# Performance work log

Measured on AMD Instinct MI355X. Metric: run time of the kernel, lower is better.

Reference implementation:

```python
import jax, jax.numpy as jnp
import numpy as np

C_M, C_Z, C, H = 256, 128, 32, 8
N_SEQ, N_RES = 256, 256
EPS = 1e-5


def _layer_norm(x, w, b):
    mu = jnp.mean(x, axis=-1, keepdims=True)
    var = jnp.mean(jnp.square(x - mu), axis=-1, keepdims=True)
    return (x - mu) * jax.lax.rsqrt(var + EPS) * w + b


def setup_inputs() -> dict:
    key = jax.random.key(0)
    ks = jax.random.split(key, 10)
    s = lambda fan_in: 1.0 / np.sqrt(fan_in)
    return {
        "m": jax.random.normal(ks[0], (N_SEQ, N_RES, C_M), jnp.float32),
        "z": jax.random.normal(ks[1], (N_RES, N_RES, C_Z), jnp.float32),
        "ln_m_w": jnp.ones((C_M,), jnp.float32),
        "ln_m_b": jnp.zeros((C_M,), jnp.float32),
        "ln_z_w": jnp.ones((C_Z,), jnp.float32),
        "ln_z_b": jnp.zeros((C_Z,), jnp.float32),
        "w_z": jax.random.normal(ks[2], (C_Z, H), jnp.float32) * s(C_Z),
        "w_q": jax.random.normal(ks[3], (C_M, H * C), jnp.float32) * s(C_M),
        "w_k": jax.random.normal(ks[4], (C_M, H * C), jnp.float32) * s(C_M),
        "w_v": jax.random.normal(ks[5], (C_M, H * C), jnp.float32) * s(C_M),
        "w_g": jax.random.normal(ks[6], (C_M, H * C), jnp.float32) * s(C_M),
        "b_g": jnp.zeros((H * C,), jnp.float32),
        "w_o": jax.random.normal(ks[7], (H * C, C_M), jnp.float32) * s(H * C),
        "b_o": jnp.zeros((C_M,), jnp.float32),
    }


def reference(m, z, ln_m_w, ln_m_b, ln_z_w, ln_z_b, w_z, w_q, w_k, w_v, w_g, b_g, w_o, b_o):
    S, R = m.shape[0], m.shape[1]
    mn = _layer_norm(m, ln_m_w, ln_m_b)                      # (S, R, c_m)
    # pair bias: LN + Linear(c_z -> H), then movedim(-1, -3): (R, R, H) -> (H, R, R)
    bias = jnp.moveaxis(_layer_norm(z, ln_z_w, ln_z_b) @ w_z, -1, -3)

    q = (mn @ w_q).reshape(S, R, H, C)
    k = (mn @ w_k).reshape(S, R, H, C)
    v = (mn @ w_v).reshape(S, R, H, C)

    scale = 1.0 / np.sqrt(C)
    # attention over residue axis (attn_dim=-2); bias broadcast over N_seq
    logits = jnp.einsum("sqhd,skhd->shqk", q, k) * scale + bias[None]  # (S, H, R, R)
    attn = jax.nn.softmax(logits, axis=-1)
    o = jnp.einsum("shqk,skhd->sqhd", attn, v).reshape(S, R, H * C)

    g = jax.nn.sigmoid(mn @ w_g + b_g)                       # (S, R, H*c)
    return (g * o) @ w_o + b_o                               # (S, R, c_m)
```

## Files before the change

kernel.cpp:

```cpp
#include <hip/hip_runtime.h>
#include <hip/hip_bf16.h>

typedef __hip_bfloat16 bf16;
typedef __attribute__((ext_vector_type(8))) short short8;
typedef __attribute__((ext_vector_type(16))) float f32x16;

#define NS 256
#define NR 256
#define CM 256
#define CZ 128
#define NH 8
#define CH 32
#define LN_EPS 1e-5f
#define LOG2E 1.4426950408889634f
#define SCALE2 (0.17677669529663687f * 1.4426950408889634f)

__device__ __forceinline__ unsigned pk_bf16(float lo, float hi) {
  unsigned r;
  asm volatile("v_cvt_pk_bf16_f32 %0, %1, %2" : "=v"(r) : "v"(lo), "v"(hi));
  return r;
}

__device__ __forceinline__ short8 load8(const bf16* p) {
  return __builtin_bit_cast(short8, *(const uint4*)p);
}

__global__ __launch_bounds__(256) void pack_w_kernel(
    const float* __restrict__ wq, const float* __restrict__ wk,
    const float* __restrict__ wv, const float* __restrict__ wg,
    const float* __restrict__ wo, bf16* __restrict__ dst) {
  int mat = blockIdx.y;
  const float* src = mat == 0 ? wq : mat == 1 ? wk : mat == 2 ? wv
                   : mat == 3 ? wg : wo;
  float sc = (mat == 0) ? SCALE2 : 1.0f;
  int t = blockIdx.x * 256 + threadIdx.x;
  int n = t & 255;
  int hi = (t >> 8) & 1;
  int kc = t >> 9;
  int kbase = kc * 16 + hi * 8;
  bf16 tmp[8];
  #pragma unroll
  for (int j = 0; j < 8; ++j)
    tmp[j] = __float2bfloat16(src[(size_t)(kbase + j) * 256 + n] * sc);
  *(uint4*)(dst + (size_t)mat * 65536 +
            ((size_t)(kc * 2 + hi) * 256 + n) * 8) = *(const uint4*)tmp;
}

__global__ __launch_bounds__(256) void ln_m_kernel(
    const float* __restrict__ m, const float* __restrict__ w,
    const float* __restrict__ b, bf16* __restrict__ mn) {
  int row = blockIdx.x * 4 + (threadIdx.x >> 6);
  int lane = threadIdx.x & 63;

  float4 x = ((const float4*)(m + (size_t)row * CM))[lane];
  float sum = x.x + x.y + x.z + x.w;
  #pragma unroll
  for (int off = 32; off; off >>= 1) sum += __shfl_xor(sum, off);
  float mu = sum * (1.0f / CM);

  float dx = x.x - mu, dy = x.y - mu, dz = x.z - mu, dw = x.w - mu;
  float ss = dx * dx + dy * dy + dz * dz + dw * dw;
  #pragma unroll
  for (int off = 32; off; off >>= 1) ss += __shfl_xor(ss, off);
  float rs = rsqrtf(ss * (1.0f / CM) + LN_EPS);

  float4 wv = ((const float4*)w)[lane];
  float4 bv = ((const float4*)b)[lane];
  unsigned p0 = pk_bf16(dx * rs * wv.x + bv.x, dy * rs * wv.y + bv.y);
  unsigned p1 = pk_bf16(dz * rs * wv.z + bv.z, dw * rs * wv.w + bv.w);
  uint2 u;
  u.x = p0;
  u.y = p1;
  *(uint2*)(mn + (size_t)row * CM + lane * 4) = u;
}

__global__ __launch_bounds__(128) void bias_kernel(
    const float* __restrict__ z, const float* __restrict__ w,
    const float* __restrict__ b, const float* __restrict__ wz,
    float* __restrict__ biasP) {
  int row = blockIdx.x;
  int t = threadIdx.x;
  __shared__ float red[2];
  __shared__ float zn[CZ];
  __shared__ float part[16][9];

  float x = z[(size_t)row * CZ + t];

  float v = x;
  #pragma unroll
  for (int off = 32; off; off >>= 1) v += __shfl_xor(v, off);
  if ((t & 63) == 0) red[t >> 6] = v;
  __syncthreads();
  float mu = (red[0] + red[1]) * (1.0f / CZ);
  float d = x - mu;
  __syncthreads();

  v = d * d;
  #pragma unroll
  for (int off = 32; off; off >>= 1) v += __shfl_xor(v, off);
  if ((t & 63) == 0) red[t >> 6] = v;
  __syncthreads();
  float var = (red[0] + red[1]) * (1.0f / CZ);

  zn[t] = d * rsqrtf(var + LN_EPS) * w[t] + b[t];
  __syncthreads();

  int h = t & 7, grp = t >> 3;
  float acc = 0.0f;
  #pragma unroll
  for (int cc = 0; cc < 8; ++cc) {
    int c = grp * 8 + cc;
    acc += zn[c] * wz[c * NH + h];
  }
  part[grp][h] = acc;
  __syncthreads();

  if (t < NH) {
    float s = 0.0f;
    #pragma unroll
    for (int g = 0; g < 16; ++g) s += part[g][t];
    int i = row >> 8, j = row & 255;
    int qt = i >> 5, lo = i & 31;
    int tt = j >> 5, rem = j & 31;
    int hi2 = (rem >> 2) & 1;
    int r = ((rem >> 3) << 2) | (rem & 3);
    biasP[(((size_t)t * 8 + qt) * 128 + tt * 16 + r) * 64 + hi2 * 32 + lo] =
        s * LOG2E;
  }
}

__global__ __launch_bounds__(256, 2) void qkvg_mfma_kernel(
    const bf16* __restrict__ mn, const bf16* __restrict__ wp,
    const float* __restrict__ bg,
    bf16* __restrict__ qo, bf16* __restrict__ ko,
    bf16* __restrict__ vo, bf16* __restrict__ go) {
  int mat = threadIdx.x >> 6;
  int lane = threadIdx.x & 63;
  int lo = lane & 31, hi = lane >> 5;
  size_t m0 = (size_t)blockIdx.x * 32;

  const bf16* arow = mn + (m0 + lo) * 256 + hi * 8;
  const bf16* wbase = wp + (size_t)mat * 65536 + ((size_t)hi * 256 + lo) * 8;

  f32x16 acc[8] = {};
  #pragma unroll 2
  for (int kc = 0; kc < 16; ++kc) {
    short8 a = load8(arow + kc * 16);
    const bf16* wkc = wbase + (size_t)kc * 4096;
    #pragma unroll
    for (int nt = 0; nt < 8; ++nt) {
      short8 b = load8(wkc + nt * 256);
      acc[nt] = __builtin_amdgcn_mfma_f32_32x32x16_bf16(a, b, acc[nt], 0, 0, 0);
    }
  }

  bf16* outp = mat == 0 ? qo : mat == 1 ? ko : mat == 2 ? vo : go;
  if (mat == 3) {
    #pragma unroll
    for (int nt = 0; nt < 8; ++nt) {
      float bgv = bg[nt * 32 + lo];
      #pragma unroll
      for (int r = 0; r < 16; ++r) {
        int crow = (r & 3) + ((r >> 2) << 3) + (hi << 2);
        float sv = 1.0f / (1.0f + __expf(-(acc[nt][r] + bgv)));
        outp[(m0 + crow) * 256 + nt * 32 + lo] = __float2bfloat16(sv);
      }
    }
  } else {
    #pragma unroll
    for (int nt = 0; nt < 8; ++nt) {
      #pragma unroll
      for (int r = 0; r < 16; ++r) {
        int crow = (r & 3) + ((r >> 2) << 3) + (hi << 2);
        outp[(m0 + crow) * 256 + nt * 32 + lo] = __float2bfloat16(acc[nt][r]);
      }
    }
  }
}

__global__ __launch_bounds__(256) void transpose_v_kernel(
    const bf16* __restrict__ vo, bf16* __restrict__ vT) {
  int s = blockIdx.x >> 3, h = blockIdx.x & 7;
  int t = threadIdx.x;
  __shared__ bf16 tile[256][40];

  #pragma unroll
  for (int p = 0; p < 4; ++p) {
    int k = p * 64 + (t >> 2);
    int c0 = (t & 3) * 8;
    uint4 u = *(const uint4*)(vo + ((size_t)(s * 256 + k)) * 256 + h * 32 + c0);
    *(uint4*)&tile[k][c0] = u;
  }
  __syncthreads();

  int c = t >> 3, k0 = (t & 7) * 32;
  bf16 buf[32];
  #pragma unroll
  for (int j = 0; j < 32; ++j) buf[j] = tile[k0 + j][c];
  bf16* dst = vT + (((size_t)(s * 8 + h) * 32 + c) * 256 + k0);
  #pragma unroll
  for (int q = 0; q < 4; ++q)
    *(uint4*)(dst + q * 8) = *(const uint4*)(buf + q * 8);
}

__global__ __launch_bounds__(256, 2) void attn_mfma_kernel(
    const bf16* __restrict__ qb, const bf16* __restrict__ kb,
    const bf16* __restrict__ vT, const bf16* __restrict__ gb,
    const float* __restrict__ biasP, bf16* __restrict__ gob) {
  int wb = (blockIdx.x & 7) * 512 + (blockIdx.x >> 3);
  int wid = wb * 4 + (threadIdx.x >> 6);
  int lane = threadIdx.x & 63;
  int lo = lane & 31;
  int hi = lane >> 5;
  int s = wid >> 6;
  int h = (wid >> 3) & 7;
  int qt = wid & 7;
  int q0 = qt * 32;

  const size_t base = (size_t)s * NR * 256 + h * CH;

  const float* bp = biasP + (((size_t)h * 8 + qt) * 128) * 64 + lane;

  short8 qf[2];
  #pragma unroll
  for (int cc = 0; cc < 2; ++cc)
    qf[cc] = load8(qb + base + (size_t)(q0 + lo) * 256 + cc * 16 + hi * 8);

  f32x16 acc[8];
  __builtin_amdgcn_s_setprio(1);
  #pragma unroll
  for (int t = 0; t < 8; ++t) {
    short8 kf0 = load8(kb + base + (size_t)(t * 32 + lo) * 256 + hi * 8);
    short8 kf1 = load8(kb + base + (size_t)(t * 32 + lo) * 256 + 16 + hi * 8);
    f32x16 z = {};
    acc[t] = __builtin_amdgcn_mfma_f32_32x32x16_bf16(kf0, qf[0], z, 0, 0, 0);
    acc[t] = __builtin_amdgcn_mfma_f32_32x32x16_bf16(kf1, qf[1], acc[t], 0, 0, 0);
  }
  __builtin_amdgcn_s_setprio(0);

  float l0 = 0.0f, l1 = 0.0f, l2 = 0.0f, l3 = 0.0f;
  #pragma unroll
  for (int t = 0; t < 8; ++t) {
    #pragma unroll
    for (int r = 0; r < 16; r += 4) {
      float e0 = exp2f(acc[t][r + 0] + bp[(t * 16 + r + 0) * 64]);
      float e1 = exp2f(acc[t][r + 1] + bp[(t * 16 + r + 1) * 64]);
      float e2 = exp2f(acc[t][r + 2] + bp[(t * 16 + r + 2) * 64]);
      float e3 = exp2f(acc[t][r + 3] + bp[(t * 16 + r + 3) * 64]);
      acc[t][r + 0] = e0;
      acc[t][r + 1] = e1;
      acc[t][r + 2] = e2;
      acc[t][r + 3] = e3;
      l0 += e0;
      l1 += e1;
      l2 += e2;
      l3 += e3;
    }
  }
  float l = (l0 + l1) + (l2 + l3);
  l += __shfl_xor(l, 32);

  f32x16 o = {};
  const bf16* vt = vT + ((size_t)(s * NH + h) * CH + lo) * 256;
  #pragma unroll
  for (int kc = 0; kc < 16; ++kc) {
    int t = kc >> 1;
    int rb = (kc & 1) << 3;
    unsigned uL0 = pk_bf16(acc[t][rb + 0], acc[t][rb + 1]);
    unsigned uL1 = pk_bf16(acc[t][rb + 2], acc[t][rb + 3]);
    unsigned uH0 = pk_bf16(acc[t][rb + 4], acc[t][rb + 5]);
    unsigned uH1 = pk_bf16(acc[t][rb + 6], acc[t][rb + 7]);
    unsigned sL0 = __shfl_xor(uL0, 32), sL1 = __shfl_xor(uL1, 32);
    unsigned sH0 = __shfl_xor(uH0, 32), sH1 = __shfl_xor(uH1, 32);
    uint4 pu;
    pu.x = hi ? sH0 : uL0;
    pu.y = hi ? sH1 : uL1;
    pu.z = hi ? uH0 : sL0;
    pu.w = hi ? uH1 : sL1;
    short8 pf = __builtin_bit_cast(short8, pu);
    short8 vf = load8(vt + kc * 16 + hi * 8);
    o = __builtin_amdgcn_mfma_f32_32x32x16_bf16(pf, vf, o, 0, 0, 0);
  }

  float linv = 1.0f / l;
  #pragma unroll
  for (int r = 0; r < 16; ++r) {
    int crow = (r & 3) + ((r >> 2) << 3) + (hi << 2);
    float li = __shfl(linv, crow);
    size_t idx = base + (size_t)(q0 + crow) * 256 + lo;
    float gg = __bfloat162float(gb[idx]);
    gob[idx] = __float2bfloat16(gg * o[r] * li);
  }
}

__global__ __launch_bounds__(256, 2) void out_mfma_kernel(
    const bf16* __restrict__ gob, const bf16* __restrict__ wop,
    const float* __restrict__ bo, float* __restrict__ out) {
  int wid = blockIdx.x * 4 + (threadIdx.x >> 6);
  int lane = threadIdx.x & 63;
  int lo = lane & 31, hi = lane >> 5;
  size_t m0 = (size_t)wid * 32;

  const bf16* arow = gob + (m0 + lo) * 256 + hi * 8;
  const bf16* wbase = wop + ((size_t)hi * 256 + lo) * 8;

  f32x16 acc[8] = {};
  #pragma unroll 2
  for (int kc = 0; kc < 16; ++kc) {
    short8 a = load8(arow + kc * 16);
    const bf16* wkc = wbase + (size_t)kc * 4096;
    #pragma unroll
    for (int nt = 0; nt < 8; ++nt) {
      short8 b = load8(wkc + nt * 256);
      acc[nt] = __builtin_amdgcn_mfma_f32_32x32x16_bf16(a, b, acc[nt], 0, 0, 0);
    }
  }

  #pragma unroll
  for (int nt = 0; nt < 8; ++nt) {
    float bv = bo[nt * 32 + lo];
    #pragma unroll
    for (int r = 0; r < 16; ++r) {
      int crow = (r & 3) + ((r >> 2) << 3) + (hi << 2);
      out[(m0 + crow) * 256 + nt * 32 + lo] = acc[nt][r] + bv;
    }
  }
}

extern "C" void kernel_launch(void* const* d_in, const int* in_sizes, int n_in,
                              void* d_out, int out_size, void* d_ws, size_t ws_size,
                              hipStream_t stream) {
  const float* m      = (const float*)d_in[0];
  const float* z      = (const float*)d_in[1];
  const float* ln_m_w = (const float*)d_in[2];
  const float* ln_m_b = (const float*)d_in[3];
  const float* ln_z_w = (const float*)d_in[4];
  const float* ln_z_b = (const float*)d_in[5];
  const float* w_z    = (const float*)d_in[6];
  const float* w_q    = (const float*)d_in[7];
  const float* w_k    = (const float*)d_in[8];
  const float* w_v    = (const float*)d_in[9];
  const float* w_g    = (const float*)d_in[10];
  const float* b_g    = (const float*)d_in[11];
  const float* w_o    = (const float*)d_in[12];
  const float* b_o    = (const float*)d_in[13];
  float* out = (float*)d_out;

  const size_t SZ = (size_t)NS * NR * 256;

  bf16* mn   = (bf16*)d_ws;
  bf16* qb   = mn + SZ;
  bf16* kb   = qb + SZ;
  bf16* vo   = kb + SZ;
  bf16* gb   = vo + SZ;
  bf16* gob  = gb + SZ;
  float* biasP = (float*)(gob + SZ);
  bf16* wp   = (bf16*)(biasP + NH * NR * NR);
  bf16* wop  = wp + 4 * 65536;
  bf16* vT   = mn;

  pack_w_kernel<<<dim3(32, 5), 256, 0, stream>>>(w_q, w_k, w_v, w_g, w_o, wp);
  ln_m_kernel<<<(NS * NR) / 4, 256, 0, stream>>>(m, ln_m_w, ln_m_b, mn);
  bias_kernel<<<NR * NR, 128, 0, stream>>>(z, ln_z_w, ln_z_b, w_z, biasP);
  qkvg_mfma_kernel<<<(NS * NR) / 32, 256, 0, stream>>>(mn, wp, b_g,
                                                       qb, kb, vo, gb);
  transpose_v_kernel<<<NS * NH, 256, 0, stream>>>(vo, vT);
  attn_mfma_kernel<<<(NS * NH * 8) / 4, 256, 0, stream>>>(qb, kb, vT, gb,
                                                          biasP, gob);
  out_mfma_kernel<<<(NS * NR) / 32 / 4, 256, 0, stream>>>(gob, wop, b_o, out);
}
```

Before: 311.6 us.

## Split attention into two key halves, vectorize bias loads, raise occupancy

```diff
diff --git a/kernel.cpp b/kernel.cpp
--- a/kernel.cpp
+++ b/kernel.cpp
@@ -124,8 +124,10 @@
     int tt = j >> 5, rem = j & 31;
     int hi2 = (rem >> 2) & 1;
     int r = ((rem >> 3) << 2) | (rem & 3);
-    biasP[(((size_t)t * 8 + qt) * 128 + tt * 16 + r) * 64 + hi2 * 32 + lo] =
-        s * LOG2E;
+    int ifrag = tt * 16 + r;
+    int lane = hi2 * 32 + lo;
+    biasP[((((size_t)t * 8 + qt) * 32 + (ifrag >> 2)) * 64 + lane) * 4 +
+          (ifrag & 3)] = s * LOG2E;
   }
 }
 
@@ -203,7 +205,7 @@
     *(uint4*)(dst + q * 8) = *(const uint4*)(buf + q * 8);
 }
 
-__global__ __launch_bounds__(256, 2) void attn_mfma_kernel(
+__global__ __launch_bounds__(256, 3) void attn_mfma_kernel(
     const bf16* __restrict__ qb, const bf16* __restrict__ kb,
     const bf16* __restrict__ vT, const bf16* __restrict__ gb,
     const float* __restrict__ biasP, bf16* __restrict__ gob) {
@@ -219,70 +221,81 @@
 
   const size_t base = (size_t)s * NR * 256 + h * CH;
 
-  const float* bp = biasP + (((size_t)h * 8 + qt) * 128) * 64 + lane;
+  const float4* bp4 =
+      (const float4*)biasP + ((size_t)(h * 8 + qt) * 32) * 64 + lane;
 
   short8 qf[2];
   #pragma unroll
   for (int cc = 0; cc < 2; ++cc)
     qf[cc] = load8(qb + base + (size_t)(q0 + lo) * 256 + cc * 16 + hi * 8);
 
-  f32x16 acc[8];
-  __builtin_amdgcn_s_setprio(1);
-  #pragma unroll
-  for (int t = 0; t < 8; ++t) {
-    short8 kf0 = load8(kb + base + (size_t)(t * 32 + lo) * 256 + hi * 8);
-    short8 kf1 = load8(kb + base + (size_t)(t * 32 + lo) * 256 + 16 + hi * 8);
-    f32x16 z = {};
-    acc[t] = __builtin_amdgcn_mfma_f32_32x32x16_bf16(kf0, qf[0], z, 0, 0, 0);
-    acc[t] = __builtin_amdgcn_mfma_f32_32x32x16_bf16(kf1, qf[1], acc[t], 0, 0, 0);
-  }
-  __builtin_amdgcn_s_setprio(0);
-
+  const bf16* vt = vT + ((size_t)(s * NH + h) * CH + lo) * 256;
+
+  f32x16 o = {};
   float l0 = 0.0f, l1 = 0.0f, l2 = 0.0f, l3 = 0.0f;
-  #pragma unroll
-  for (int t = 0; t < 8; ++t) {
-    #pragma unroll
-    for (int r = 0; r < 16; r += 4) {
-      float e0 = exp2f(acc[t][r + 0] + bp[(t * 16 + r + 0) * 64]);
-      float e1 = exp2f(acc[t][r + 1] + bp[(t * 16 + r + 1) * 64]);
-      float e2 = exp2f(acc[t][r + 2] + bp[(t * 16 + r + 2) * 64]);
-      float e3 = exp2f(acc[t][r + 3] + bp[(t * 16 + r + 3) * 64]);
-      acc[t][r + 0] = e0;
-      acc[t][r + 1] = e1;
-      acc[t][r + 2] = e2;
-      acc[t][r + 3] = e3;
-      l0 += e0;
-      l1 += e1;
-      l2 += e2;
-      l3 += e3;
-    }
-  }
+
+  #pragma unroll
+  for (int hs = 0; hs < 2; ++hs) {
+    f32x16 acc[4];
+    __builtin_amdgcn_s_setprio(1);
+    #pragma unroll
+    for (int th = 0; th < 4; ++th) {
+      int t = hs * 4 + th;
+      short8 kf0 = load8(kb + base + (size_t)(t * 32 + lo) * 256 + hi * 8);
+      short8 kf1 = load8(kb + base + (size_t)(t * 32 + lo) * 256 + 16 + hi * 8);
+      f32x16 z = {};
+      acc[th] = __builtin_amdgcn_mfma_f32_32x32x16_bf16(kf0, qf[0], z, 0, 0, 0);
+      acc[th] =
+          __builtin_amdgcn_mfma_f32_32x32x16_bf16(kf1, qf[1], acc[th], 0, 0, 0);
+    }
+    __builtin_amdgcn_s_setprio(0);
+
+    #pragma unroll
+    for (int th = 0; th < 4; ++th) {
+      int t = hs * 4 + th;
+      #pragma unroll
+      for (int j = 0; j < 4; ++j) {
+        float4 b4 = bp4[(t * 4 + j) * 64];
+        float e0 = exp2f(acc[th][j * 4 + 0] + b4.x);
+        float e1 = exp2f(acc[th][j * 4 + 1] + b4.y);
+        float e2 = exp2f(acc[th][j * 4 + 2] + b4.z);
+        float e3 = exp2f(acc[th][j * 4 + 3] + b4.w);
+        acc[th][j * 4 + 0] = e0;
+        acc[th][j * 4 + 1] = e1;
+        acc[th][j * 4 + 2] = e2;
+        acc[th][j * 4 + 3] = e3;
+        l0 += e0;
+        l1 += e1;
+        l2 += e2;
+        l3 += e3;
+      }
+    }
+
+    #pragma unroll
+    for (int kc2 = 0; kc2 < 8; ++kc2) {
+      int th = kc2 >> 1;
+      int rb = (kc2 & 1) << 3;
+      unsigned uL0 = pk_bf16(acc[th][rb + 0], acc[th][rb + 1]);
+      unsigned uL1 = pk_bf16(acc[th][rb + 2], acc[th][rb + 3]);
+      unsigned uH0 = pk_bf16(acc[th][rb + 4], acc[th][rb + 5]);
+      unsigned uH1 = pk_bf16(acc[th][rb + 6], acc[th][rb + 7]);
+      unsigned sL0 = __shfl_xor(uL0, 32), sL1 = __shfl_xor(uL1, 32);
+      unsigned sH0 = __shfl_xor(uH0, 32), sH1 = __shfl_xor(uH1, 32);
+      uint4 pu;
+      pu.x = hi ? sH0 : uL0;
+      pu.y = hi ? sH1 : uL1;
+      pu.z = hi ? uH0 : sL0;
+      pu.w = hi ? uH1 : sL1;
+      short8 pf = __builtin_bit_cast(short8, pu);
+      short8 vf = load8(vt + (hs * 8 + kc2) * 16 + hi * 8);
+      o = __builtin_amdgcn_mfma_f32_32x32x16_bf16(pf, vf, o, 0, 0, 0);
+    }
+  }
+
   float l = (l0 + l1) + (l2 + l3);
   l += __shfl_xor(l, 32);
-
-  f32x16 o = {};
-  const bf16* vt = vT + ((size_t)(s * NH + h) * CH + lo) * 256;
-  #pragma unroll
-  for (int kc = 0; kc < 16; ++kc) {
-    int t = kc >> 1;
-    int rb = (kc & 1) << 3;
-    unsigned uL0 = pk_bf16(acc[t][rb + 0], acc[t][rb + 1]);
-    unsigned uL1 = pk_bf16(acc[t][rb + 2], acc[t][rb + 3]);
-    unsigned uH0 = pk_bf16(acc[t][rb + 4], acc[t][rb + 5]);
-    unsigned uH1 = pk_bf16(acc[t][rb + 6], acc[t][rb + 7]);
-    unsigned sL0 = __shfl_xor(uL0, 32), sL1 = __shfl_xor(uL1, 32);
-    unsigned sH0 = __shfl_xor(uH0, 32), sH1 = __shfl_xor(uH1, 32);
-    uint4 pu;
-    pu.x = hi ? sH0 : uL0;
-    pu.y = hi ? sH1 : uL1;
-    pu.z = hi ? uH0 : sL0;
-    pu.w = hi ? uH1 : sL1;
-    short8 pf = __builtin_bit_cast(short8, pu);
-    short8 vf = load8(vt + kc * 16 + hi * 8);
-    o = __builtin_amdgcn_mfma_f32_32x32x16_bf16(pf, vf, o, 0, 0, 0);
-  }
-
   float linv = 1.0f / l;
+
   #pragma unroll
   for (int r = 0; r < 16; ++r) {
     int crow = (r & 3) + ((r >> 2) << 3) + (hi << 2);
```

Result: faster. 299.3 us (-4.0%).
